# Performance work log

Hardware: AMD Instinct MI355X
Metric: run time of the kernel (lower is better)

Reference implementation:

```python
import jax, jax.numpy as jnp
import numpy as np
import math

CHANNELS = 512
N_HEADS = 8
K_CH = CHANNELS // N_HEADS            # 64 per-head dim
ROPE_D = int(K_CH * 0.5)              # 32 dims get RoPE, rest pass through
BASE = 10000


def _rope(x):
    # x: [b, h, t, dk]; rotate first ROPE_D dims (half-split style, matching the torch module)
    d = ROPE_D
    t = x.shape[2]
    theta = 1.0 / (BASE ** (jnp.arange(0, d, 2, dtype=jnp.float32) / d))      # [d/2]
    ang = jnp.arange(t, dtype=jnp.float32)[:, None] * theta[None, :]          # [t, d/2]
    ang = jnp.concatenate([ang, ang], axis=-1)                                # [t, d]
    cos = jnp.cos(ang)[None, None, :, :].astype(x.dtype)
    sin = jnp.sin(ang)[None, None, :, :].astype(x.dtype)
    x_rope, x_pass = x[..., :d], x[..., d:]
    neg_half = jnp.concatenate([-x_rope[..., d // 2:], x_rope[..., :d // 2]], axis=-1)
    return jnp.concatenate([x_rope * cos + neg_half * sin, x_pass], axis=-1)


def _split_heads(y):
    # [b, (h c), t] -> [b, h, t, c]
    b, _, t = y.shape
    return y.reshape(b, N_HEADS, K_CH, t).transpose(0, 1, 3, 2)


def setup_inputs() -> dict:
    key = jax.random.key(0)
    ks = jax.random.split(key, 10)
    B, T = 8, 1024
    w_scale = 1.0 / math.sqrt(CHANNELS)
    return {
        "x": jax.random.normal(ks[0], (B, CHANNELS, T), jnp.float32),
        "c": jax.random.normal(ks[1], (B, CHANNELS, T), jnp.float32),
        "Wq": jax.random.normal(ks[2], (CHANNELS, CHANNELS), jnp.float32) * w_scale,
        "bq": jax.random.normal(ks[3], (CHANNELS,), jnp.float32) * 0.02,
        "Wk": jax.random.normal(ks[4], (CHANNELS, CHANNELS), jnp.float32) * w_scale,
        "bk": jax.random.normal(ks[5], (CHANNELS,), jnp.float32) * 0.02,
        "Wv": jax.random.normal(ks[6], (CHANNELS, CHANNELS), jnp.float32) * w_scale,
        "bv": jax.random.normal(ks[7], (CHANNELS,), jnp.float32) * 0.02,
        "Wo": jax.random.normal(ks[8], (CHANNELS, CHANNELS), jnp.float32) * w_scale,
        "bo": jax.random.normal(ks[9], (CHANNELS,), jnp.float32) * 0.02,
    }


def reference(x, c, Wq, bq, Wk, bk, Wv, bv, Wo, bo):
    # 1x1 Conv1d == per-timestep linear over channels
    q = jnp.einsum('oc,bct->bot', Wq, x) + bq[None, :, None]
    k = jnp.einsum('oc,bct->bot', Wk, c) + bk[None, :, None]
    v = jnp.einsum('oc,bct->bot', Wv, c) + bv[None, :, None]

    q = _rope(_split_heads(q))            # [b,h,t,ck]
    k = _rope(_split_heads(k))            # [b,h,s,ck]
    v = _split_heads(v)                   # [b,h,s,ck]

    scale = 1.0 / math.sqrt(K_CH)
    scores = jnp.einsum('bhtc,bhsc->bhts', q, k) * scale
    p_attn = jax.nn.softmax(scores, axis=-1)       # dropout p=0 -> identity
    out = jnp.einsum('bhts,bhsc->bhtc', p_attn, v)

    b, _, t, _ = out.shape
    out = out.transpose(0, 1, 3, 2).reshape(b, CHANNELS, t)   # [b, (h c), t]
    return jnp.einsum('oc,bct->bot', Wo, out) + bo[None, :, None]
```

## Files before the change

### kernel.cpp

```cpp
#include <hip/hip_runtime.h>

typedef __bf16 bf16x8 __attribute__((ext_vector_type(8)));
typedef float  f32x4  __attribute__((ext_vector_type(4)));

__device__ __forceinline__ unsigned short f2bf(float f){
    union { float f; unsigned u; } v; v.f = f;
    v.u += 0x7fffu + ((v.u >> 16) & 1u);
    return (unsigned short)(v.u >> 16);
}
__device__ __forceinline__ void gl2lds16(const unsigned short* g, unsigned short* l){
    __builtin_amdgcn_global_load_lds(
        (const __attribute__((address_space(1))) void*)g,
        (__attribute__((address_space(3))) void*)l, 16, 0, 0);
}

__global__ __launch_bounds__(256) void transpose_cvt(const float* __restrict__ x, const float* __restrict__ c,
                                                     const float* __restrict__ w0, const float* __restrict__ w1,
                                                     const float* __restrict__ w2, const float* __restrict__ w3,
                                                     unsigned short* __restrict__ xt, unsigned short* __restrict__ ct,
                                                     unsigned short* __restrict__ o0, unsigned short* __restrict__ o1,
                                                     unsigned short* __restrict__ o2, unsigned short* __restrict__ o3){
    __shared__ float tile[64][72];
    const int z = blockIdx.z;
    if (z == 16){
        int fid = (blockIdx.x * 8 + blockIdx.y) * 256 + threadIdx.x;
        const float* in; unsigned short* out;
        switch (fid >> 13){
            case 0: in = w0; out = o0; break;
            case 1: in = w1; out = o1; break;
            case 2: in = w2; out = o2; break;
            default: in = w3; out = o3; break;
        }
        int off = (fid & 8191) * 32;
        #pragma unroll
        for (int j = 0; j < 8; j++){
            float4 v = *(const float4*)(in + off + j*4);
            ushort4 o; o.x = f2bf(v.x); o.y = f2bf(v.y); o.z = f2bf(v.z); o.w = f2bf(v.w);
            *(ushort4*)(out + off + j*4) = o;
        }
        return;
    }
    const float* in = (z < 8) ? x : c;
    unsigned short* out = (z < 8) ? xt : ct;
    const int b = z & 7;
    const int t0 = blockIdx.x * 64, c0 = blockIdx.y * 64;
    const int tid = threadIdx.x;
    {
        int r = tid >> 2, q = (tid & 3) * 16;
        const float* src = in + ((size_t)b * 512 + c0 + r) * 1024 + t0 + q;
        #pragma unroll
        for (int j = 0; j < 4; j++)
            *(float4*)&tile[r][q + j*4] = ((const float4*)src)[j];
    }
    __syncthreads();
    {
        int tr = tid >> 2, cj = (tid & 3) * 16;
        unsigned pw[8];
        #pragma unroll
        for (int j = 0; j < 8; j++){
            unsigned lo = f2bf(tile[cj + 2*j    ][tr]);
            unsigned hi = f2bf(tile[cj + 2*j + 1][tr]);
            pw[j] = lo | (hi << 16);
        }
        unsigned short* dst = out + ((size_t)b * 1024 + t0 + tr) * 512 + c0 + cj;
        uint4 q0 = {pw[0], pw[1], pw[2], pw[3]};
        uint4 q1 = {pw[4], pw[5], pw[6], pw[7]};
        ((uint4*)dst)[0] = q0;
        ((uint4*)dst)[1] = q1;
    }
}

__device__ __forceinline__ void gemm_mainloop(const unsigned short* __restrict__ A,
                                              const unsigned short* __restrict__ Bm,
                                              unsigned short* a_s, unsigned short* b_s,
                                              int m0, int n0, int tid, f32x4 acc[4][4]){
    const int wave = tid >> 6, lane = tid & 63;
    const int l15 = lane & 15, l4 = lane >> 4;
    const int mw = (wave >> 1) * 64, nw = (wave & 1) * 64;
    const int r8 = lane >> 3, c8l = lane & 7;
    const int csw = (c8l ^ r8) * 8;
    const int rp = l15 & 7;

    auto stage = [&](int k0, int buf){
        unsigned short* as = a_s + buf * (128*64);
        unsigned short* bs = b_s + buf * (128*64);
        #pragma unroll
        for (int i = 0; i < 4; i++){
            int rg = i * 4 + wave;
            int row = rg * 8 + r8;
            gl2lds16(A  + (size_t)(m0 + row) * 512 + k0 + csw, as + rg * 512);
            gl2lds16(Bm + (size_t)(n0 + row) * 512 + k0 + csw, bs + rg * 512);
        }
    };

    stage(0, 0);
    __syncthreads();

    for (int t = 0; t < 8; t++){
        const int buf = t & 1;
        if (t < 7) stage((t + 1) * 64, buf ^ 1);
        const unsigned short* as = a_s + buf * (128*64);
        const unsigned short* bs = b_s + buf * (128*64);
        #pragma unroll
        for (int kk = 0; kk < 2; kk++){
            bf16x8 af[4], bfr[4];
            #pragma unroll
            for (int mt = 0; mt < 4; mt++)
                af[mt] = *(const bf16x8*)&as[(mw + mt*16 + l15)*64 + (((kk*4) + l4) ^ rp)*8];
            #pragma unroll
            for (int ct = 0; ct < 4; ct++)
                bfr[ct] = *(const bf16x8*)&bs[(nw + ct*16 + l15)*64 + (((kk*4) + l4) ^ rp)*8];
            #pragma unroll
            for (int mt = 0; mt < 4; mt++)
                #pragma unroll
                for (int ct = 0; ct < 4; ct++)
                    acc[mt][ct] = __builtin_amdgcn_mfma_f32_16x16x32_bf16(
                        af[mt], bfr[ct], acc[mt][ct], 0, 0, 0);
        }
        __syncthreads();
    }
}

__global__ __launch_bounds__(256) void qkv_gemm(const unsigned short* __restrict__ xt,
                                                const unsigned short* __restrict__ ct,
                                                const unsigned short* __restrict__ wq,
                                                const unsigned short* __restrict__ wk,
                                                const unsigned short* __restrict__ wv,
                                                const float* __restrict__ bq_,
                                                const float* __restrict__ bk_,
                                                const float* __restrict__ bv_,
                                                unsigned short* __restrict__ qt,
                                                unsigned short* __restrict__ kt,
                                                unsigned short* __restrict__ vct){
    __shared__ unsigned short a_s[2*128*64];
    __shared__ unsigned short b_s[2*128*64];
    const int z = blockIdx.y;
    const int xr = blockIdx.x;
    const int bid = (xr & 7) * 32 + (xr >> 3);
    const unsigned short *A, *Bm;
    int m0, n0;
    if (z == 0){ A = xt; Bm = wq; m0 = (bid >> 2)*128; n0 = (bid & 3)*128; }
    else if (z == 1){ A = ct; Bm = wk; m0 = (bid >> 2)*128; n0 = (bid & 3)*128; }
    else { A = wv; Bm = ct; m0 = (bid & 3)*128; n0 = (bid >> 2)*128; }
    const int tid = threadIdx.x;
    const int wave = tid >> 6, lane = tid & 63;
    const int l15 = lane & 15, l4 = lane >> 4;
    const int mw = (wave >> 1) * 64, nw = (wave & 1) * 64;
    const f32x4 vzero = {0.f, 0.f, 0.f, 0.f};
    f32x4 acc[4][4];
    #pragma unroll
    for (int i = 0; i < 4; i++)
        #pragma unroll
        for (int j = 0; j < 4; j++) acc[i][j] = vzero;

    gemm_mainloop(A, Bm, a_s, b_s, m0, n0, tid, acc);

    if (z < 2){
        unsigned short* out = (z == 0) ? qt : kt;
        const float* bias = (z == 0) ? bq_ : bk_;
        const float osc = (z == 0) ? 0.1803368801111137f : 1.0f;
        float bv4[4];
        #pragma unroll
        for (int ct2 = 0; ct2 < 4; ct2++) bv4[ct2] = bias[n0 + nw + ct2*16 + l15];
        const float theta = __powf(10000.0f, -(float)l15 * (1.0f / 16.0f));
        #pragma unroll
        for (int mt = 0; mt < 4; mt++){
            #pragma unroll
            for (int rr = 0; rr < 4; rr++){
                int row = m0 + mw + mt*16 + l4*4 + rr;
                int t = row & 1023;
                float v[4];
                #pragma unroll
                for (int ct2 = 0; ct2 < 4; ct2++) v[ct2] = acc[mt][ct2][rr] + bv4[ct2];
                float sn, cn;
                __sincosf((float)t * theta, &sn, &cn);
                float r0 = v[0] * cn - v[1] * sn;
                float r1 = v[1] * cn + v[0] * sn;
                v[0] = r0; v[1] = r1;
                #pragma unroll
                for (int ct2 = 0; ct2 < 4; ct2++)
                    out[(size_t)row * 512 + n0 + nw + ct2*16 + l15] = f2bf(v[ct2] * osc);
            }
        }
    } else {
        #pragma unroll
        for (int mt = 0; mt < 4; mt++){
            #pragma unroll
            for (int rr = 0; rr < 4; rr++){
                int row = m0 + mw + mt*16 + l4*4 + rr;
                float bb = bv_[row];
                #pragma unroll
                for (int ct2 = 0; ct2 < 4; ct2++){
                    int n = n0 + nw + ct2*16 + l15;
                    size_t oaddr = (size_t)(n >> 10) * 524288 + (size_t)row * 1024 + (n & 1023);
                    vct[oaddr] = f2bf(acc[mt][ct2][rr] + bb);
                }
            }
        }
    }
}

__global__ __launch_bounds__(256) void gemm_o(const unsigned short* __restrict__ wo,
                                              const unsigned short* __restrict__ attnT,
                                              const float* __restrict__ bo,
                                              float* __restrict__ out){
    __shared__ unsigned short a_s[2*64*64];
    __shared__ unsigned short b_s[2*128*64];
    const int m0 = blockIdx.x * 64, n0 = blockIdx.y * 128;
    const int tid = threadIdx.x;
    const int wave = tid >> 6, lane = tid & 63;
    const int l15 = lane & 15, l4 = lane >> 4;
    const int nw = wave * 32;
    const int r8 = lane >> 3, c8l = lane & 7;
    const int csw = (c8l ^ r8) * 8;
    const int rp = l15 & 7;
    const f32x4 vzero = {0.f, 0.f, 0.f, 0.f};
    f32x4 acc[4][2];
    #pragma unroll
    for (int i = 0; i < 4; i++){ acc[i][0] = vzero; acc[i][1] = vzero; }

    auto stage = [&](int k0, int buf){
        unsigned short* as = a_s + buf * (64*64);
        unsigned short* bs = b_s + buf * (128*64);
        #pragma unroll
        for (int i = 0; i < 2; i++){
            int rg = wave * 2 + i;
            gl2lds16(wo + (size_t)(m0 + rg*8 + r8) * 512 + k0 + csw, as + rg * 512);
        }
        #pragma unroll
        for (int i = 0; i < 4; i++){
            int rg = wave * 4 + i;
            gl2lds16(attnT + (size_t)(n0 + rg*8 + r8) * 512 + k0 + csw, bs + rg * 512);
        }
    };

    stage(0, 0);
    __syncthreads();

    for (int t = 0; t < 8; t++){
        const int buf = t & 1;
        if (t < 7) stage((t + 1) * 64, buf ^ 1);
        const unsigned short* as = a_s + buf * (64*64);
        const unsigned short* bs = b_s + buf * (128*64);
        #pragma unroll
        for (int kk = 0; kk < 2; kk++){
            bf16x8 af[4], bfr[2];
            #pragma unroll
            for (int mt = 0; mt < 4; mt++)
                af[mt] = *(const bf16x8*)&as[(mt*16 + l15)*64 + (((kk*4) + l4) ^ rp)*8];
            #pragma unroll
            for (int ct = 0; ct < 2; ct++)
                bfr[ct] = *(const bf16x8*)&bs[(nw + ct*16 + l15)*64 + (((kk*4) + l4) ^ rp)*8];
            #pragma unroll
            for (int mt = 0; mt < 4; mt++)
                #pragma unroll
                for (int ct = 0; ct < 2; ct++)
                    acc[mt][ct] = __builtin_amdgcn_mfma_f32_16x16x32_bf16(
                        af[mt], bfr[ct], acc[mt][ct], 0, 0, 0);
        }
        __syncthreads();
    }

    #pragma unroll
    for (int mt = 0; mt < 4; mt++){
        #pragma unroll
        for (int rr = 0; rr < 4; rr++){
            int row = m0 + mt*16 + l4*4 + rr;
            float bb = bo[row];
            #pragma unroll
            for (int ct2 = 0; ct2 < 2; ct2++){
                int n = n0 + nw + ct2*16 + l15;
                size_t oaddr = (size_t)(n >> 10) * 524288 + (size_t)row * 1024 + (n & 1023);
                out[oaddr] = acc[mt][ct2][rr] + bb;
            }
        }
    }
}

__global__ __launch_bounds__(256, 2) void flash_attn(const unsigned short* __restrict__ qt,
                                                     const unsigned short* __restrict__ kt,
                                                     const unsigned short* __restrict__ vct,
                                                     unsigned short* __restrict__ attnT){
    __shared__ unsigned short k_s[2][64*64];
    __shared__ unsigned short v_s[2][64*64];
    __shared__ unsigned short p_s[4][2][16*72];
    const int bhq = blockIdx.x;
    const int bh = bhq & 63, b = bh >> 3, h = bh & 7;
    const int q0 = (bhq >> 6) * 128;
    const int tid = threadIdx.x, wave = tid >> 6, lane = tid & 63;
    const int l15 = lane & 15, l4 = lane >> 4;
    const int r8 = lane >> 3, c8l = lane & 7;
    const int csw = (c8l ^ r8) * 8;
    const int rp = l15 & 7;
    const f32x4 vzero = {0.f, 0.f, 0.f, 0.f};
    const unsigned short* kbase = kt  + (size_t)(b*1024)*512 + h*64;
    const unsigned short* vbase = vct + (size_t)(b*512 + h*64)*1024;

    bf16x8 qf[2][2];
    #pragma unroll
    for (int st = 0; st < 2; st++)
        #pragma unroll
        for (int kh = 0; kh < 2; kh++)
            qf[st][kh] = *(const bf16x8*)(qt + (size_t)(b*1024 + q0 + wave*32 + st*16 + l15)*512
                                             + h*64 + kh*32 + l4*8);
    f32x4 o_acc[2][4], l_acc[2];
    #pragma unroll
    for (int st = 0; st < 2; st++){
        l_acc[st] = vzero;
        #pragma unroll
        for (int dt = 0; dt < 4; dt++) o_acc[st][dt] = vzero;
    }
    const __bf16 one_bf = (__bf16)1.0f;
    const bf16x8 ones = {one_bf, one_bf, one_bf, one_bf, one_bf, one_bf, one_bf, one_bf};

    auto stage = [&](int tile, int buf){
        const int s0n = tile * 64;
        #pragma unroll
        for (int i = 0; i < 2; i++){
            int rg = i * 4 + wave;
            int row = rg * 8 + r8;
            gl2lds16(kbase + (size_t)(s0n + row)*512 + csw, &k_s[buf][rg*512]);
            gl2lds16(vbase + (size_t)row*1024 + s0n + csw, &v_s[buf][rg*512]);
        }
    };
    stage(0, 0);
    __syncthreads();

    for (int it = 0; it < 16; ++it){
        const int cur = it & 1;
        if (it < 15) stage(it + 1, cur ^ 1);
        bf16x8 kf[2][4], vf[2][4];
        #pragma unroll
        for (int kh = 0; kh < 2; kh++)
            #pragma unroll
            for (int ct = 0; ct < 4; ct++)
                kf[kh][ct] = *(const bf16x8*)&k_s[cur][(ct*16 + l15)*64 + ((kh*4 + l4) ^ rp)*8];
        #pragma unroll
        for (int sh = 0; sh < 2; sh++)
            #pragma unroll
            for (int dt = 0; dt < 4; dt++)
                vf[sh][dt] = *(const bf16x8*)&v_s[cur][(dt*16 + l15)*64 + ((sh*4 + l4) ^ rp)*8];
        #pragma unroll
        for (int st = 0; st < 2; st++){
            f32x4 sa[4];
            #pragma unroll
            for (int ct = 0; ct < 4; ct++) sa[ct] = vzero;
            #pragma unroll
            for (int kh = 0; kh < 2; kh++)
                #pragma unroll
                for (int ct = 0; ct < 4; ct++)
                    sa[ct] = __builtin_amdgcn_mfma_f32_16x16x32_bf16(kf[kh][ct], qf[st][kh], sa[ct], 0, 0, 0);
            #pragma unroll
            for (int ct = 0; ct < 4; ct++)
                #pragma unroll
                for (int rr = 0; rr < 4; rr++)
                    sa[ct][rr] = exp2f(sa[ct][rr]);
            #pragma unroll
            for (int ct = 0; ct < 4; ct++){
                union { float f; unsigned u; } a0, a1, a2, a3;
                a0.f = sa[ct][0]; a1.f = sa[ct][1]; a2.f = sa[ct][2]; a3.f = sa[ct][3];
                uint2 w;
                w.x = (a0.u >> 16) | (a1.u & 0xffff0000u);
                w.y = (a2.u >> 16) | (a3.u & 0xffff0000u);
                *(uint2*)&p_s[wave][st][l15*72 + ct*16 + l4*4] = w;
            }
            asm volatile("s_waitcnt lgkmcnt(0)" ::: "memory");
            __builtin_amdgcn_sched_barrier(0);
            bf16x8 ap0 = *(const bf16x8*)&p_s[wave][st][l15*72 + l4*8];
            bf16x8 ap1 = *(const bf16x8*)&p_s[wave][st][l15*72 + 32 + l4*8];
            l_acc[st] = __builtin_amdgcn_mfma_f32_16x16x32_bf16(ap0, ones, l_acc[st], 0, 0, 0);
            l_acc[st] = __builtin_amdgcn_mfma_f32_16x16x32_bf16(ap1, ones, l_acc[st], 0, 0, 0);
            #pragma unroll
            for (int dt = 0; dt < 4; dt++){
                o_acc[st][dt] = __builtin_amdgcn_mfma_f32_16x16x32_bf16(ap0, vf[0][dt], o_acc[st][dt], 0, 0, 0);
                o_acc[st][dt] = __builtin_amdgcn_mfma_f32_16x16x32_bf16(ap1, vf[1][dt], o_acc[st][dt], 0, 0, 0);
            }
        }
        __syncthreads();
    }
    #pragma unroll
    for (int st = 0; st < 2; st++){
        float rl[4];
        #pragma unroll
        for (int rr = 0; rr < 4; rr++) rl[rr] = __builtin_amdgcn_rcpf(l_acc[st][rr]);
        #pragma unroll
        for (int dt = 0; dt < 4; dt++)
            #pragma unroll
            for (int rr = 0; rr < 4; rr++){
                int row = q0 + wave*32 + st*16 + l4*4 + rr;
                attnT[(size_t)(b*1024 + row)*512 + h*64 + dt*16 + l15] = f2bf(o_acc[st][dt][rr] * rl[rr]);
            }
    }
}

extern "C" void kernel_launch(void* const* d_in, const int* in_sizes, int n_in,
                              void* d_out, int out_size, void* d_ws, size_t ws_size,
                              hipStream_t stream){
    const float* x  = (const float*)d_in[0];
    const float* c  = (const float*)d_in[1];
    const float* Wq = (const float*)d_in[2];
    const float* bq = (const float*)d_in[3];
    const float* Wk = (const float*)d_in[4];
    const float* bk = (const float*)d_in[5];
    const float* Wv = (const float*)d_in[6];
    const float* bv = (const float*)d_in[7];
    const float* Wo = (const float*)d_in[8];
    const float* bo = (const float*)d_in[9];

    unsigned short* wq_b = (unsigned short*)d_ws;
    unsigned short* wk_b = wq_b + 262144;
    unsigned short* wv_b = wk_b + 262144;
    unsigned short* wo_b = wv_b + 262144;
    unsigned short* xt   = wo_b + 262144;
    unsigned short* ct   = xt  + 4194304;
    unsigned short* qt   = ct  + 4194304;
    unsigned short* kt   = qt  + 4194304;
    unsigned short* vct  = kt  + 4194304;
    unsigned short* attnT = xt;

    transpose_cvt<<<dim3(16, 8, 17), 256, 0, stream>>>(x, c, Wq, Wk, Wv, Wo,
                                                       xt, ct, wq_b, wk_b, wv_b, wo_b);
    qkv_gemm<<<dim3(256, 3), 256, 0, stream>>>(xt, ct, wq_b, wk_b, wv_b, bq, bk, bv, qt, kt, vct);
    flash_attn<<<dim3(512), 256, 0, stream>>>(qt, kt, vct, attnT);
    gemm_o<<<dim3(8, 64), 256, 0, stream>>>(wo_b, attnT, bo, (float*)d_out);
}
```

Baseline: 164.6 us.

## Fuse all four stages into one persistent cooperative kernel with grid syncs

Replaces the four separate launches (transpose/convert, QKV GEMM, flash attention, output GEMM) with a single persistent cooperative kernel. Work units of each stage are looped over by 512 (or 256) blocks, with grid-wide synchronisation between stages. The aim is to remove inter-kernel launch gaps and tail drain. In exchange it adds grid-sync cost, a shared 64KB LDS buffer that may limit occupancy, and a fallback to the original four launches if the cooperative launch fails.

```diff
diff --git a/kernel.cpp b/kernel.cpp
--- a/kernel.cpp
+++ b/kernel.cpp
@@ -1,4 +1,6 @@
 #include <hip/hip_runtime.h>
+#include <hip/hip_cooperative_groups.h>
+namespace cg = cooperative_groups;
 
 typedef __bf16 bf16x8 __attribute__((ext_vector_type(8)));
 typedef float  f32x4  __attribute__((ext_vector_type(4)));
@@ -12,62 +14,6 @@
     __builtin_amdgcn_global_load_lds(
         (const __attribute__((address_space(1))) void*)g,
         (__attribute__((address_space(3))) void*)l, 16, 0, 0);
-}
-
-__global__ __launch_bounds__(256) void transpose_cvt(const float* __restrict__ x, const float* __restrict__ c,
-                                                     const float* __restrict__ w0, const float* __restrict__ w1,
-                                                     const float* __restrict__ w2, const float* __restrict__ w3,
-                                                     unsigned short* __restrict__ xt, unsigned short* __restrict__ ct,
-                                                     unsigned short* __restrict__ o0, unsigned short* __restrict__ o1,
-                                                     unsigned short* __restrict__ o2, unsigned short* __restrict__ o3){
-    __shared__ float tile[64][72];
-    const int z = blockIdx.z;
-    if (z == 16){
-        int fid = (blockIdx.x * 8 + blockIdx.y) * 256 + threadIdx.x;
-        const float* in; unsigned short* out;
-        switch (fid >> 13){
-            case 0: in = w0; out = o0; break;
-            case 1: in = w1; out = o1; break;
-            case 2: in = w2; out = o2; break;
-            default: in = w3; out = o3; break;
-        }
-        int off = (fid & 8191) * 32;
-        #pragma unroll
-        for (int j = 0; j < 8; j++){
-            float4 v = *(const float4*)(in + off + j*4);
-            ushort4 o; o.x = f2bf(v.x); o.y = f2bf(v.y); o.z = f2bf(v.z); o.w = f2bf(v.w);
-            *(ushort4*)(out + off + j*4) = o;
-        }
-        return;
-    }
-    const float* in = (z < 8) ? x : c;
-    unsigned short* out = (z < 8) ? xt : ct;
-    const int b = z & 7;
-    const int t0 = blockIdx.x * 64, c0 = blockIdx.y * 64;
-    const int tid = threadIdx.x;
-    {
-        int r = tid >> 2, q = (tid & 3) * 16;
-        const float* src = in + ((size_t)b * 512 + c0 + r) * 1024 + t0 + q;
-        #pragma unroll
-        for (int j = 0; j < 4; j++)
-            *(float4*)&tile[r][q + j*4] = ((const float4*)src)[j];
-    }
-    __syncthreads();
-    {
-        int tr = tid >> 2, cj = (tid & 3) * 16;
-        unsigned pw[8];
-        #pragma unroll
-        for (int j = 0; j < 8; j++){
-            unsigned lo = f2bf(tile[cj + 2*j    ][tr]);
-            unsigned hi = f2bf(tile[cj + 2*j + 1][tr]);
-            pw[j] = lo | (hi << 16);
-        }
-        unsigned short* dst = out + ((size_t)b * 1024 + t0 + tr) * 512 + c0 + cj;
-        uint4 q0 = {pw[0], pw[1], pw[2], pw[3]};
-        uint4 q1 = {pw[4], pw[5], pw[6], pw[7]};
-        ((uint4*)dst)[0] = q0;
-        ((uint4*)dst)[1] = q1;
-    }
 }
 
 __device__ __forceinline__ void gemm_mainloop(const unsigned short* __restrict__ A,
@@ -119,6 +65,378 @@
         }
         __syncthreads();
     }
+}
+
+__device__ __forceinline__ void do_transpose_unit(int u, int tid, unsigned char* smem,
+        const float* x, const float* c, const float* Wq, const float* Wk,
+        const float* Wv, const float* Wo,
+        unsigned short* xt, unsigned short* ct,
+        unsigned short* wq_b, unsigned short* wk_b,
+        unsigned short* wv_b, unsigned short* wo_b){
+    const int bz = u >> 7, rem = u & 127;
+    if (bz == 16){
+        int fid = rem * 256 + tid;
+        const float* in; unsigned short* outp;
+        switch (fid >> 13){
+            case 0: in = Wq; outp = wq_b; break;
+            case 1: in = Wk; outp = wk_b; break;
+            case 2: in = Wv; outp = wv_b; break;
+            default: in = Wo; outp = wo_b; break;
+        }
+        int off = (fid & 8191) * 32;
+        #pragma unroll
+        for (int j = 0; j < 8; j++){
+            float4 v = *(const float4*)(in + off + j*4);
+            ushort4 o; o.x = f2bf(v.x); o.y = f2bf(v.y); o.z = f2bf(v.z); o.w = f2bf(v.w);
+            *(ushort4*)(outp + off + j*4) = o;
+        }
+    } else {
+        float (*tile)[72] = (float(*)[72])smem;
+        const float* in = (bz < 8) ? x : c;
+        unsigned short* outp = (bz < 8) ? xt : ct;
+        const int b = bz & 7;
+        const int t0 = (rem >> 3) * 64, c0 = (rem & 7) * 64;
+        {
+            int r = tid >> 2, q = (tid & 3) * 16;
+            const float* src = in + ((size_t)b * 512 + c0 + r) * 1024 + t0 + q;
+            #pragma unroll
+            for (int j = 0; j < 4; j++)
+                *(float4*)&tile[r][q + j*4] = ((const float4*)src)[j];
+        }
+        __syncthreads();
+        {
+            int tr = tid >> 2, cj = (tid & 3) * 16;
+            unsigned pw[8];
+            #pragma unroll
+            for (int j = 0; j < 8; j++){
+                unsigned lo = f2bf(tile[cj + 2*j    ][tr]);
+                unsigned hi = f2bf(tile[cj + 2*j + 1][tr]);
+                pw[j] = lo | (hi << 16);
+            }
+            unsigned short* dst = outp + ((size_t)b * 1024 + t0 + tr) * 512 + c0 + cj;
+            uint4 q0 = {pw[0], pw[1], pw[2], pw[3]};
+            uint4 q1 = {pw[4], pw[5], pw[6], pw[7]};
+            ((uint4*)dst)[0] = q0;
+            ((uint4*)dst)[1] = q1;
+        }
+    }
+}
+
+__device__ __forceinline__ void do_qkv_unit(int u, int tid, unsigned char* smem,
+        const unsigned short* xt, const unsigned short* ct,
+        const unsigned short* wq_b, const unsigned short* wk_b, const unsigned short* wv_b,
+        const float* bq, const float* bk, const float* bv,
+        unsigned short* qt, unsigned short* kt, unsigned short* vct){
+    unsigned short* a_s = (unsigned short*)smem;
+    unsigned short* b_s = a_s + 2*128*64;
+    const int wave = tid >> 6, lane = tid & 63;
+    const int l15 = lane & 15, l4 = lane >> 4;
+    const int z = u >> 8, xr = u & 255;
+    const int bid2 = (xr & 7) * 32 + (xr >> 3);
+    const unsigned short *A, *Bm;
+    int m0, n0;
+    if (z == 0){ A = xt; Bm = wq_b; m0 = (bid2 >> 2)*128; n0 = (bid2 & 3)*128; }
+    else if (z == 1){ A = ct; Bm = wk_b; m0 = (bid2 >> 2)*128; n0 = (bid2 & 3)*128; }
+    else { A = wv_b; Bm = ct; m0 = (bid2 & 3)*128; n0 = (bid2 >> 2)*128; }
+    const int mw = (wave >> 1) * 64, nw = (wave & 1) * 64;
+    const f32x4 vzero = {0.f, 0.f, 0.f, 0.f};
+    f32x4 acc[4][4];
+    #pragma unroll
+    for (int i = 0; i < 4; i++)
+        #pragma unroll
+        for (int j = 0; j < 4; j++) acc[i][j] = vzero;
+
+    gemm_mainloop(A, Bm, a_s, b_s, m0, n0, tid, acc);
+
+    if (z < 2){
+        unsigned short* outp = (z == 0) ? qt : kt;
+        const float* bias = (z == 0) ? bq : bk;
+        const float osc = (z == 0) ? 0.1803368801111137f : 1.0f;
+        float bv4[4];
+        #pragma unroll
+        for (int ct2 = 0; ct2 < 4; ct2++) bv4[ct2] = bias[n0 + nw + ct2*16 + l15];
+        const float theta = __powf(10000.0f, -(float)l15 * (1.0f / 16.0f));
+        #pragma unroll
+        for (int mt = 0; mt < 4; mt++){
+            #pragma unroll
+            for (int rr = 0; rr < 4; rr++){
+                int row = m0 + mw + mt*16 + l4*4 + rr;
+                int t = row & 1023;
+                float v[4];
+                #pragma unroll
+                for (int ct2 = 0; ct2 < 4; ct2++) v[ct2] = acc[mt][ct2][rr] + bv4[ct2];
+                float sn, cn;
+                __sincosf((float)t * theta, &sn, &cn);
+                float r0 = v[0] * cn - v[1] * sn;
+                float r1 = v[1] * cn + v[0] * sn;
+                v[0] = r0; v[1] = r1;
+                #pragma unroll
+                for (int ct2 = 0; ct2 < 4; ct2++)
+                    outp[(size_t)row * 512 + n0 + nw + ct2*16 + l15] = f2bf(v[ct2] * osc);
+            }
+        }
+    } else {
+        #pragma unroll
+        for (int mt = 0; mt < 4; mt++){
+            #pragma unroll
+            for (int rr = 0; rr < 4; rr++){
+                int row = m0 + mw + mt*16 + l4*4 + rr;
+                float bb = bv[row];
+                #pragma unroll
+                for (int ct2 = 0; ct2 < 4; ct2++){
+                    int n = n0 + nw + ct2*16 + l15;
+                    size_t oaddr = (size_t)(n >> 10) * 524288 + (size_t)row * 1024 + (n & 1023);
+                    vct[oaddr] = f2bf(acc[mt][ct2][rr] + bb);
+                }
+            }
+        }
+    }
+}
+
+__device__ __forceinline__ void do_flash_unit(int u, int tid, unsigned char* smem,
+        const unsigned short* qt, const unsigned short* kt, const unsigned short* vct,
+        unsigned short* attnT){
+    unsigned short* k_s = (unsigned short*)smem;
+    unsigned short* v_s = k_s + 2*64*64;
+    unsigned short* p_s = v_s + 2*64*64;
+    const int wave = tid >> 6, lane = tid & 63;
+    const int l15 = lane & 15, l4 = lane >> 4;
+    const int r8 = lane >> 3, c8l = lane & 7;
+    const int csw = (c8l ^ r8) * 8;
+    const int rp = l15 & 7;
+    const f32x4 vzero = {0.f, 0.f, 0.f, 0.f};
+    const int bh = u & 63, b = bh >> 3, h = bh & 7;
+    const int q0 = (u >> 6) * 128;
+    const unsigned short* kbase = kt  + (size_t)(b*1024)*512 + h*64;
+    const unsigned short* vbase = vct + (size_t)(b*512 + h*64)*1024;
+
+    bf16x8 qf[2][2];
+    #pragma unroll
+    for (int st = 0; st < 2; st++)
+        #pragma unroll
+        for (int kh = 0; kh < 2; kh++)
+            qf[st][kh] = *(const bf16x8*)(qt + (size_t)(b*1024 + q0 + wave*32 + st*16 + l15)*512
+                                             + h*64 + kh*32 + l4*8);
+    f32x4 o_acc[2][4], l_acc[2];
+    #pragma unroll
+    for (int st = 0; st < 2; st++){
+        l_acc[st] = vzero;
+        #pragma unroll
+        for (int dt = 0; dt < 4; dt++) o_acc[st][dt] = vzero;
+    }
+    const __bf16 one_bf = (__bf16)1.0f;
+    const bf16x8 ones = {one_bf, one_bf, one_bf, one_bf, one_bf, one_bf, one_bf, one_bf};
+
+    auto stage = [&](int tile, int buf){
+        const int s0n = tile * 64;
+        #pragma unroll
+        for (int i = 0; i < 2; i++){
+            int rg = i * 4 + wave;
+            int row = rg * 8 + r8;
+            gl2lds16(kbase + (size_t)(s0n + row)*512 + csw, &k_s[buf*4096 + rg*512]);
+            gl2lds16(vbase + (size_t)row*1024 + s0n + csw, &v_s[buf*4096 + rg*512]);
+        }
+    };
+    stage(0, 0);
+    __syncthreads();
+
+    for (int it = 0; it < 16; ++it){
+        const int cur = it & 1;
+        if (it < 15) stage(it + 1, cur ^ 1);
+        bf16x8 kf[2][4], vf[2][4];
+        #pragma unroll
+        for (int kh = 0; kh < 2; kh++)
+            #pragma unroll
+            for (int ct = 0; ct < 4; ct++)
+                kf[kh][ct] = *(const bf16x8*)&k_s[cur*4096 + (ct*16 + l15)*64 + ((kh*4 + l4) ^ rp)*8];
+        #pragma unroll
+        for (int sh = 0; sh < 2; sh++)
+            #pragma unroll
+            for (int dt = 0; dt < 4; dt++)
+                vf[sh][dt] = *(const bf16x8*)&v_s[cur*4096 + (dt*16 + l15)*64 + ((sh*4 + l4) ^ rp)*8];
+        #pragma unroll
+        for (int st = 0; st < 2; st++){
+            f32x4 sa[4];
+            #pragma unroll
+            for (int ct = 0; ct < 4; ct++) sa[ct] = vzero;
+            #pragma unroll
+            for (int kh = 0; kh < 2; kh++)
+                #pragma unroll
+                for (int ct = 0; ct < 4; ct++)
+                    sa[ct] = __builtin_amdgcn_mfma_f32_16x16x32_bf16(kf[kh][ct], qf[st][kh], sa[ct], 0, 0, 0);
+            #pragma unroll
+            for (int ct = 0; ct < 4; ct++)
+                #pragma unroll
+                for (int rr = 0; rr < 4; rr++)
+                    sa[ct][rr] = exp2f(sa[ct][rr]);
+            unsigned short* ps = p_s + ((wave << 1) + st) * (16*72);
+            #pragma unroll
+            for (int ct = 0; ct < 4; ct++){
+                union { float f; unsigned u; } a0, a1, a2, a3;
+                a0.f = sa[ct][0]; a1.f = sa[ct][1]; a2.f = sa[ct][2]; a3.f = sa[ct][3];
+                uint2 w;
+                w.x = (a0.u >> 16) | (a1.u & 0xffff0000u);
+                w.y = (a2.u >> 16) | (a3.u & 0xffff0000u);
+                *(uint2*)&ps[l15*72 + ct*16 + l4*4] = w;
+            }
+            asm volatile("s_waitcnt lgkmcnt(0)" ::: "memory");
+            __builtin_amdgcn_sched_barrier(0);
+            bf16x8 ap0 = *(const bf16x8*)&ps[l15*72 + l4*8];
+            bf16x8 ap1 = *(const bf16x8*)&ps[l15*72 + 32 + l4*8];
+            l_acc[st] = __builtin_amdgcn_mfma_f32_16x16x32_bf16(ap0, ones, l_acc[st], 0, 0, 0);
+            l_acc[st] = __builtin_amdgcn_mfma_f32_16x16x32_bf16(ap1, ones, l_acc[st], 0, 0, 0);
+            #pragma unroll
+            for (int dt = 0; dt < 4; dt++){
+                o_acc[st][dt] = __builtin_amdgcn_mfma_f32_16x16x32_bf16(ap0, vf[0][dt], o_acc[st][dt], 0, 0, 0);
+                o_acc[st][dt] = __builtin_amdgcn_mfma_f32_16x16x32_bf16(ap1, vf[1][dt], o_acc[st][dt], 0, 0, 0);
+            }
+        }
+        __syncthreads();
+    }
+    #pragma unroll
+    for (int st = 0; st < 2; st++){
+        float rl[4];
+        #pragma unroll
+        for (int rr = 0; rr < 4; rr++) rl[rr] = __builtin_amdgcn_rcpf(l_acc[st][rr]);
+        #pragma unroll
+        for (int dt = 0; dt < 4; dt++)
+            #pragma unroll
+            for (int rr = 0; rr < 4; rr++){
+                int row = q0 + wave*32 + st*16 + l4*4 + rr;
+                attnT[(size_t)(b*1024 + row)*512 + h*64 + dt*16 + l15] = f2bf(o_acc[st][dt][rr] * rl[rr]);
+            }
+    }
+}
+
+__device__ __forceinline__ void do_out_unit(int u, int tid, unsigned char* smem,
+        const unsigned short* wo_b, const unsigned short* attnT,
+        const float* bo, float* out){
+    unsigned short* a_s = (unsigned short*)smem;
+    unsigned short* b_s = a_s + 2*64*64;
+    const int wave = tid >> 6, lane = tid & 63;
+    const int l15 = lane & 15, l4 = lane >> 4;
+    const int r8 = lane >> 3, c8l = lane & 7;
+    const int csw = (c8l ^ r8) * 8;
+    const int rp = l15 & 7;
+    const f32x4 vzero = {0.f, 0.f, 0.f, 0.f};
+    const int m0 = (u & 7) * 64, n0 = (u >> 3) * 128;
+    const int nw = wave * 32;
+    f32x4 acc[4][2];
+    #pragma unroll
+    for (int i = 0; i < 4; i++){ acc[i][0] = vzero; acc[i][1] = vzero; }
+
+    auto stage = [&](int k0, int buf){
+        unsigned short* as = a_s + buf * (64*64);
+        unsigned short* bs = b_s + buf * (128*64);
+        #pragma unroll
+        for (int i = 0; i < 2; i++){
+            int rg = wave * 2 + i;
+            gl2lds16(wo_b + (size_t)(m0 + rg*8 + r8) * 512 + k0 + csw, as + rg * 512);
+        }
+        #pragma unroll
+        for (int i = 0; i < 4; i++){
+            int rg = wave * 4 + i;
+            gl2lds16(attnT + (size_t)(n0 + rg*8 + r8) * 512 + k0 + csw, bs + rg * 512);
+        }
+    };
+
+    stage(0, 0);
+    __syncthreads();
+
+    for (int t = 0; t < 8; t++){
+        const int buf = t & 1;
+        if (t < 7) stage((t + 1) * 64, buf ^ 1);
+        const unsigned short* as = a_s + buf * (64*64);
+        const unsigned short* bs = b_s + buf * (128*64);
+        #pragma unroll
+        for (int kk = 0; kk < 2; kk++){
+            bf16x8 af[4], bfr[2];
+            #pragma unroll
+            for (int mt = 0; mt < 4; mt++)
+                af[mt] = *(const bf16x8*)&as[(mt*16 + l15)*64 + (((kk*4) + l4) ^ rp)*8];
+            #pragma unroll
+            for (int ct = 0; ct < 2; ct++)
+                bfr[ct] = *(const bf16x8*)&bs[(nw + ct*16 + l15)*64 + (((kk*4) + l4) ^ rp)*8];
+            #pragma unroll
+            for (int mt = 0; mt < 4; mt++)
+                #pragma unroll
+                for (int ct = 0; ct < 2; ct++)
+                    acc[mt][ct] = __builtin_amdgcn_mfma_f32_16x16x32_bf16(
+                        af[mt], bfr[ct], acc[mt][ct], 0, 0, 0);
+        }
+        __syncthreads();
+    }
+
+    #pragma unroll
+    for (int mt = 0; mt < 4; mt++){
+        #pragma unroll
+        for (int rr = 0; rr < 4; rr++){
+            int row = m0 + mt*16 + l4*4 + rr;
+            float bb = bo[row];
+            #pragma unroll
+            for (int ct2 = 0; ct2 < 2; ct2++){
+                int n = n0 + nw + ct2*16 + l15;
+                size_t oaddr = (size_t)(n >> 10) * 524288 + (size_t)row * 1024 + (n & 1023);
+                out[oaddr] = acc[mt][ct2][rr] + bb;
+            }
+        }
+    }
+}
+
+__global__ __launch_bounds__(256, 2) void fused_mha(
+        const float* __restrict__ x,  const float* __restrict__ c,
+        const float* __restrict__ Wq, const float* __restrict__ bq,
+        const float* __restrict__ Wk, const float* __restrict__ bk,
+        const float* __restrict__ Wv, const float* __restrict__ bv,
+        const float* __restrict__ Wo, const float* __restrict__ bo,
+        unsigned short* __restrict__ ws, float* __restrict__ out){
+    __shared__ __align__(16) unsigned char smem[65536];
+    unsigned short* wq_b = ws;
+    unsigned short* wk_b = wq_b + 262144;
+    unsigned short* wv_b = wk_b + 262144;
+    unsigned short* wo_b = wv_b + 262144;
+    unsigned short* xt   = wo_b + 262144;
+    unsigned short* ct   = xt  + 4194304;
+    unsigned short* qt   = ct  + 4194304;
+    unsigned short* kt   = qt  + 4194304;
+    unsigned short* vct  = kt  + 4194304;
+    unsigned short* attnT = xt;
+
+    const int bid = blockIdx.x, tid = threadIdx.x, G = gridDim.x;
+
+    for (int u = bid; u < 2176; u += G){
+        do_transpose_unit(u, tid, smem, x, c, Wq, Wk, Wv, Wo, xt, ct, wq_b, wk_b, wv_b, wo_b);
+        __syncthreads();
+    }
+    __threadfence();
+    cg::this_grid().sync();
+    __threadfence();
+
+    for (int u = bid; u < 768; u += G)
+        do_qkv_unit(u, tid, smem, xt, ct, wq_b, wk_b, wv_b, bq, bk, bv, qt, kt, vct);
+    __threadfence();
+    cg::this_grid().sync();
+    __threadfence();
+
+    for (int u = bid; u < 512; u += G)
+        do_flash_unit(u, tid, smem, qt, kt, vct, attnT);
+    __threadfence();
+    cg::this_grid().sync();
+    __threadfence();
+
+    for (int u = bid; u < 512; u += G)
+        do_out_unit(u, tid, smem, wo_b, attnT, bo, out);
+}
+
+__global__ __launch_bounds__(256) void transpose_cvt(const float* __restrict__ x, const float* __restrict__ c,
+                                                     const float* __restrict__ w0, const float* __restrict__ w1,
+                                                     const float* __restrict__ w2, const float* __restrict__ w3,
+                                                     unsigned short* __restrict__ xt, unsigned short* __restrict__ ct,
+                                                     unsigned short* __restrict__ o0, unsigned short* __restrict__ o1,
+                                                     unsigned short* __restrict__ o2, unsigned short* __restrict__ o3){
+    __shared__ __align__(16) unsigned char smem[64*72*4];
+    int u = blockIdx.z * 128 + blockIdx.x * 8 + blockIdx.y;
+    do_transpose_unit(u, threadIdx.x, smem, x, c, w0, w1, w2, w3, xt, ct, o0, o1, o2, o3);
 }
 
 __global__ __launch_bounds__(256) void qkv_gemm(const unsigned short* __restrict__ xt,
@@ -132,265 +450,26 @@
                                                 unsigned short* __restrict__ qt,
                                                 unsigned short* __restrict__ kt,
                                                 unsigned short* __restrict__ vct){
-    __shared__ unsigned short a_s[2*128*64];
-    __shared__ unsigned short b_s[2*128*64];
-    const int z = blockIdx.y;
-    const int xr = blockIdx.x;
-    const int bid = (xr & 7) * 32 + (xr >> 3);
-    const unsigned short *A, *Bm;
-    int m0, n0;
-    if (z == 0){ A = xt; Bm = wq; m0 = (bid >> 2)*128; n0 = (bid & 3)*128; }
-    else if (z == 1){ A = ct; Bm = wk; m0 = (bid >> 2)*128; n0 = (bid & 3)*128; }
-    else { A = wv; Bm = ct; m0 = (bid & 3)*128; n0 = (bid >> 2)*128; }
-    const int tid = threadIdx.x;
-    const int wave = tid >> 6, lane = tid & 63;
-    const int l15 = lane & 15, l4 = lane >> 4;
-    const int mw = (wave >> 1) * 64, nw = (wave & 1) * 64;
-    const f32x4 vzero = {0.f, 0.f, 0.f, 0.f};
-    f32x4 acc[4][4];
-    #pragma unroll
-    for (int i = 0; i < 4; i++)
-        #pragma unroll
-        for (int j = 0; j < 4; j++) acc[i][j] = vzero;
-
-    gemm_mainloop(A, Bm, a_s, b_s, m0, n0, tid, acc);
-
-    if (z < 2){
-        unsigned short* out = (z == 0) ? qt : kt;
-        const float* bias = (z == 0) ? bq_ : bk_;
-        const float osc = (z == 0) ? 0.1803368801111137f : 1.0f;
-        float bv4[4];
-        #pragma unroll
-        for (int ct2 = 0; ct2 < 4; ct2++) bv4[ct2] = bias[n0 + nw + ct2*16 + l15];
-        const float theta = __powf(10000.0f, -(float)l15 * (1.0f / 16.0f));
-        #pragma unroll
-        for (int mt = 0; mt < 4; mt++){
-            #pragma unroll
-            for (int rr = 0; rr < 4; rr++){
-                int row = m0 + mw + mt*16 + l4*4 + rr;
-                int t = row & 1023;
-                float v[4];
-                #pragma unroll
-                for (int ct2 = 0; ct2 < 4; ct2++) v[ct2] = acc[mt][ct2][rr] + bv4[ct2];
-                float sn, cn;
-                __sincosf((float)t * theta, &sn, &cn);
-                float r0 = v[0] * cn - v[1] * sn;
-                float r1 = v[1] * cn + v[0] * sn;
-                v[0] = r0; v[1] = r1;
-                #pragma unroll
-                for (int ct2 = 0; ct2 < 4; ct2++)
-                    out[(size_t)row * 512 + n0 + nw + ct2*16 + l15] = f2bf(v[ct2] * osc);
-            }
-        }
-    } else {
-        #pragma unroll
-        for (int mt = 0; mt < 4; mt++){
-            #pragma unroll
-            for (int rr = 0; rr < 4; rr++){
-                int row = m0 + mw + mt*16 + l4*4 + rr;
-                float bb = bv_[row];
-                #pragma unroll
-                for (int ct2 = 0; ct2 < 4; ct2++){
-                    int n = n0 + nw + ct2*16 + l15;
-                    size_t oaddr = (size_t)(n >> 10) * 524288 + (size_t)row * 1024 + (n & 1023);
-                    vct[oaddr] = f2bf(acc[mt][ct2][rr] + bb);
-                }
-            }
-        }
-    }
+    __shared__ __align__(16) unsigned char smem[65536];
+    int u = blockIdx.y * 256 + blockIdx.x;
+    do_qkv_unit(u, threadIdx.x, smem, xt, ct, wq, wk, wv, bq_, bk_, bv_, qt, kt, vct);
+}
+
+__global__ __launch_bounds__(256, 2) void flash_attn(const unsigned short* __restrict__ qt,
+                                                     const unsigned short* __restrict__ kt,
+                                                     const unsigned short* __restrict__ vct,
+                                                     unsigned short* __restrict__ attnT){
+    __shared__ __align__(16) unsigned char smem[51200];
+    do_flash_unit(blockIdx.x, threadIdx.x, smem, qt, kt, vct, attnT);
 }
 
 __global__ __launch_bounds__(256) void gemm_o(const unsigned short* __restrict__ wo,
                                               const unsigned short* __restrict__ attnT,
                                               const float* __restrict__ bo,
                                               float* __restrict__ out){
-    __shared__ unsigned short a_s[2*64*64];
-    __shared__ unsigned short b_s[2*128*64];
-    const int m0 = blockIdx.x * 64, n0 = blockIdx.y * 128;
-    const int tid = threadIdx.x;
-    const int wave = tid >> 6, lane = tid & 63;
-    const int l15 = lane & 15, l4 = lane >> 4;
-    const int nw = wave * 32;
-    const int r8 = lane >> 3, c8l = lane & 7;
-    const int csw = (c8l ^ r8) * 8;
-    const int rp = l15 & 7;
-    const f32x4 vzero = {0.f, 0.f, 0.f, 0.f};
-    f32x4 acc[4][2];
-    #pragma unroll
-    for (int i = 0; i < 4; i++){ acc[i][0] = vzero; acc[i][1] = vzero; }
-
-    auto stage = [&](int k0, int buf){
-        unsigned short* as = a_s + buf * (64*64);
-        unsigned short* bs = b_s + buf * (128*64);
-        #pragma unroll
-        for (int i = 0; i < 2; i++){
-            int rg = wave * 2 + i;
-            gl2lds16(wo + (size_t)(m0 + rg*8 + r8) * 512 + k0 + csw, as + rg * 512);
-        }
-        #pragma unroll
-        for (int i = 0; i < 4; i++){
-            int rg = wave * 4 + i;
-            gl2lds16(attnT + (size_t)(n0 + rg*8 + r8) * 512 + k0 + csw, bs + rg * 512);
-        }
-    };
-
-    stage(0, 0);
-    __syncthreads();
-
-    for (int t = 0; t < 8; t++){
-        const int buf = t & 1;
-        if (t < 7) stage((t + 1) * 64, buf ^ 1);
-        const unsigned short* as = a_s + buf * (64*64);
-        const unsigned short* bs = b_s + buf * (128*64);
-        #pragma unroll
-        for (int kk = 0; kk < 2; kk++){
-            bf16x8 af[4], bfr[2];
-            #pragma unroll
-            for (int mt = 0; mt < 4; mt++)
-                af[mt] = *(const bf16x8*)&as[(mt*16 + l15)*64 + (((kk*4) + l4) ^ rp)*8];
-            #pragma unroll
-            for (int ct = 0; ct < 2; ct++)
-                bfr[ct] = *(const bf16x8*)&bs[(nw + ct*16 + l15)*64 + (((kk*4) + l4) ^ rp)*8];
-            #pragma unroll
-            for (int mt = 0; mt < 4; mt++)
-                #pragma unroll
-                for (int ct = 0; ct < 2; ct++)
-                    acc[mt][ct] = __builtin_amdgcn_mfma_f32_16x16x32_bf16(
-                        af[mt], bfr[ct], acc[mt][ct], 0, 0, 0);
-        }
-        __syncthreads();
-    }
-
-    #pragma unroll
-    for (int mt = 0; mt < 4; mt++){
-        #pragma unroll
-        for (int rr = 0; rr < 4; rr++){
-            int row = m0 + mt*16 + l4*4 + rr;
-            float bb = bo[row];
-            #pragma unroll
-            for (int ct2 = 0; ct2 < 2; ct2++){
-                int n = n0 + nw + ct2*16 + l15;
-                size_t oaddr = (size_t)(n >> 10) * 524288 + (size_t)row * 1024 + (n & 1023);
-                out[oaddr] = acc[mt][ct2][rr] + bb;
-            }
-        }
-    }
-}
-
-__global__ __launch_bounds__(256, 2) void flash_attn(const unsigned short* __restrict__ qt,
-                                                     const unsigned short* __restrict__ kt,
-                                                     const unsigned short* __restrict__ vct,
-                                                     unsigned short* __restrict__ attnT){
-    __shared__ unsigned short k_s[2][64*64];
-    __shared__ unsigned short v_s[2][64*64];
-    __shared__ unsigned short p_s[4][2][16*72];
-    const int bhq = blockIdx.x;
-    const int bh = bhq & 63, b = bh >> 3, h = bh & 7;
-    const int q0 = (bhq >> 6) * 128;
-    const int tid = threadIdx.x, wave = tid >> 6, lane = tid & 63;
-    const int l15 = lane & 15, l4 = lane >> 4;
-    const int r8 = lane >> 3, c8l = lane & 7;
-    const int csw = (c8l ^ r8) * 8;
-    const int rp = l15 & 7;
-    const f32x4 vzero = {0.f, 0.f, 0.f, 0.f};
-    const unsigned short* kbase = kt  + (size_t)(b*1024)*512 + h*64;
-    const unsigned short* vbase = vct + (size_t)(b*512 + h*64)*1024;
-
-    bf16x8 qf[2][2];
-    #pragma unroll
-    for (int st = 0; st < 2; st++)
-        #pragma unroll
-        for (int kh = 0; kh < 2; kh++)
-            qf[st][kh] = *(const bf16x8*)(qt + (size_t)(b*1024 + q0 + wave*32 + st*16 + l15)*512
-                                             + h*64 + kh*32 + l4*8);
-    f32x4 o_acc[2][4], l_acc[2];
-    #pragma unroll
-    for (int st = 0; st < 2; st++){
-        l_acc[st] = vzero;
-        #pragma unroll
-        for (int dt = 0; dt < 4; dt++) o_acc[st][dt] = vzero;
-    }
-    const __bf16 one_bf = (__bf16)1.0f;
-    const bf16x8 ones = {one_bf, one_bf, one_bf, one_bf, one_bf, one_bf, one_bf, one_bf};
-
-    auto stage = [&](int tile, int buf){
-        const int s0n = tile * 64;
-        #pragma unroll
-        for (int i = 0; i < 2; i++){
-            int rg = i * 4 + wave;
-            int row = rg * 8 + r8;
-            gl2lds16(kbase + (size_t)(s0n + row)*512 + csw, &k_s[buf][rg*512]);
-            gl2lds16(vbase + (size_t)row*1024 + s0n + csw, &v_s[buf][rg*512]);
-        }
-    };
-    stage(0, 0);
-    __syncthreads();
-
-    for (int it = 0; it < 16; ++it){
-        const int cur = it & 1;
-        if (it < 15) stage(it + 1, cur ^ 1);
-        bf16x8 kf[2][4], vf[2][4];
-        #pragma unroll
-        for (int kh = 0; kh < 2; kh++)
-            #pragma unroll
-            for (int ct = 0; ct < 4; ct++)
-                kf[kh][ct] = *(const bf16x8*)&k_s[cur][(ct*16 + l15)*64 + ((kh*4 + l4) ^ rp)*8];
-        #pragma unroll
-        for (int sh = 0; sh < 2; sh++)
-            #pragma unroll
-            for (int dt = 0; dt < 4; dt++)
-                vf[sh][dt] = *(const bf16x8*)&v_s[cur][(dt*16 + l15)*64 + ((sh*4 + l4) ^ rp)*8];
-        #pragma unroll
-        for (int st = 0; st < 2; st++){
-            f32x4 sa[4];
-            #pragma unroll
-            for (int ct = 0; ct < 4; ct++) sa[ct] = vzero;
-            #pragma unroll
-            for (int kh = 0; kh < 2; kh++)
-                #pragma unroll
-                for (int ct = 0; ct < 4; ct++)
-                    sa[ct] = __builtin_amdgcn_mfma_f32_16x16x32_bf16(kf[kh][ct], qf[st][kh], sa[ct], 0, 0, 0);
-            #pragma unroll
-            for (int ct = 0; ct < 4; ct++)
-                #pragma unroll
-                for (int rr = 0; rr < 4; rr++)
-                    sa[ct][rr] = exp2f(sa[ct][rr]);
-            #pragma unroll
-            for (int ct = 0; ct < 4; ct++){
-                union { float f; unsigned u; } a0, a1, a2, a3;
-                a0.f = sa[ct][0]; a1.f = sa[ct][1]; a2.f = sa[ct][2]; a3.f = sa[ct][3];
-                uint2 w;
-                w.x = (a0.u >> 16) | (a1.u & 0xffff0000u);
-                w.y = (a2.u >> 16) | (a3.u & 0xffff0000u);
-                *(uint2*)&p_s[wave][st][l15*72 + ct*16 + l4*4] = w;
-            }
-            asm volatile("s_waitcnt lgkmcnt(0)" ::: "memory");
-            __builtin_amdgcn_sched_barrier(0);
-            bf16x8 ap0 = *(const bf16x8*)&p_s[wave][st][l15*72 + l4*8];
-            bf16x8 ap1 = *(const bf16x8*)&p_s[wave][st][l15*72 + 32 + l4*8];
-            l_acc[st] = __builtin_amdgcn_mfma_f32_16x16x32_bf16(ap0, ones, l_acc[st], 0, 0, 0);
-            l_acc[st] = __builtin_amdgcn_mfma_f32_16x16x32_bf16(ap1, ones, l_acc[st], 0, 0, 0);
-            #pragma unroll
-            for (int dt = 0; dt < 4; dt++){
-                o_acc[st][dt] = __builtin_amdgcn_mfma_f32_16x16x32_bf16(ap0, vf[0][dt], o_acc[st][dt], 0, 0, 0);
-                o_acc[st][dt] = __builtin_amdgcn_mfma_f32_16x16x32_bf16(ap1, vf[1][dt], o_acc[st][dt], 0, 0, 0);
-            }
-        }
-        __syncthreads();
-    }
-    #pragma unroll
-    for (int st = 0; st < 2; st++){
-        float rl[4];
-        #pragma unroll
-        for (int rr = 0; rr < 4; rr++) rl[rr] = __builtin_amdgcn_rcpf(l_acc[st][rr]);
-        #pragma unroll
-        for (int dt = 0; dt < 4; dt++)
-            #pragma unroll
-            for (int rr = 0; rr < 4; rr++){
-                int row = q0 + wave*32 + st*16 + l4*4 + rr;
-                attnT[(size_t)(b*1024 + row)*512 + h*64 + dt*16 + l15] = f2bf(o_acc[st][dt][rr] * rl[rr]);
-            }
-    }
+    __shared__ __align__(16) unsigned char smem[49152];
+    int u = blockIdx.y * 8 + blockIdx.x;
+    do_out_unit(u, threadIdx.x, smem, wo, attnT, bo, out);
 }
 
 extern "C" void kernel_launch(void* const* d_in, const int* in_sizes, int n_in,
@@ -406,21 +485,30 @@
     const float* bv = (const float*)d_in[7];
     const float* Wo = (const float*)d_in[8];
     const float* bo = (const float*)d_in[9];
-
-    unsigned short* wq_b = (unsigned short*)d_ws;
-    unsigned short* wk_b = wq_b + 262144;
-    unsigned short* wv_b = wk_b + 262144;
-    unsigned short* wo_b = wv_b + 262144;
-    unsigned short* xt   = wo_b + 262144;
-    unsigned short* ct   = xt  + 4194304;
-    unsigned short* qt   = ct  + 4194304;
-    unsigned short* kt   = qt  + 4194304;
-    unsigned short* vct  = kt  + 4194304;
-    unsigned short* attnT = xt;
-
-    transpose_cvt<<<dim3(16, 8, 17), 256, 0, stream>>>(x, c, Wq, Wk, Wv, Wo,
-                                                       xt, ct, wq_b, wk_b, wv_b, wo_b);
-    qkv_gemm<<<dim3(256, 3), 256, 0, stream>>>(xt, ct, wq_b, wk_b, wv_b, bq, bk, bv, qt, kt, vct);
-    flash_attn<<<dim3(512), 256, 0, stream>>>(qt, kt, vct, attnT);
-    gemm_o<<<dim3(8, 64), 256, 0, stream>>>(wo_b, attnT, bo, (float*)d_out);
-}
+    unsigned short* ws = (unsigned short*)d_ws;
+    float* outp = (float*)d_out;
+
+    void* args[12] = { &x, &c, &Wq, &bq, &Wk, &bk, &Wv, &bv, &Wo, &bo, &ws, &outp };
+    hipError_t e = hipLaunchCooperativeKernel((const void*)fused_mha, dim3(512), dim3(256),
+                                              args, 0, stream);
+    if (e != hipSuccess)
+        e = hipLaunchCooperativeKernel((const void*)fused_mha, dim3(256), dim3(256),
+                                       args, 0, stream);
+    if (e != hipSuccess){
+        unsigned short* wq_b = ws;
+        unsigned short* wk_b = wq_b + 262144;
+        unsigned short* wv_b = wk_b + 262144;
+        unsigned short* wo_b = wv_b + 262144;
+        unsigned short* xt   = wo_b + 262144;
+        unsigned short* ct   = xt  + 4194304;
+        unsigned short* qt   = ct  + 4194304;
+        unsigned short* kt   = qt  + 4194304;
+        unsigned short* vct  = kt  + 4194304;
+        unsigned short* attnT = xt;
+        transpose_cvt<<<dim3(16, 8, 17), 256, 0, stream>>>(x, c, Wq, Wk, Wv, Wo,
+                                                           xt, ct, wq_b, wk_b, wv_b, wo_b);
+        qkv_gemm<<<dim3(256, 3), 256, 0, stream>>>(xt, ct, wq_b, wk_b, wv_b, bq, bk, bv, qt, kt, vct);
+        flash_attn<<<dim3(512), 256, 0, stream>>>(qt, kt, vct, attnT);
+        gemm_o<<<dim3(8, 64), 256, 0, stream>>>(wo_b, attnT, bo, (float*)d_out);
+    }
+}
```

After: 633.4 us. 3.85x slower.
